# Optimization experiments

Measured on AMD Instinct MI355X. Metric: run time of the kernel, lower is better.

The kernel has to match this reference:

```python
import jax, jax.numpy as jnp
import numpy as np


def setup_inputs() -> dict:
    key = jax.random.key(0)
    kx, kc = jax.random.split(key)
    N, K, D = 32768, 4096, 512
    x = jax.random.normal(kx, (N, D), dtype=jnp.float32)
    # matches torch.rand(K, D) * 0.2 - 0.1
    codebook = jax.random.uniform(kc, (K, D), dtype=jnp.float32) * 0.2 - 0.1
    return {"x": x, "codebook": codebook}


def reference(x, codebook):
    x_sq = jnp.sum(x * x, axis=-1, keepdims=True)            # [N, 1]
    c_sq = jnp.sum(codebook * codebook, axis=-1)             # [K]
    dists = x_sq - 2.0 * jnp.einsum('nd,kd->nk', x, codebook) + c_sq[None, :]
    Z = jnp.argmin(dists, axis=-1)                           # [N] int
    q = codebook[Z]                                          # [N, D] gather
    q_with_st = x + jax.lax.stop_gradient(q - x)             # straight-through
    vq_loss = jnp.mean((jax.lax.stop_gradient(q) - x) ** 2)
    commitment_loss = jnp.mean((jax.lax.stop_gradient(x) - q) ** 2)
    return Z, q_with_st, vq_loss, commitment_loss
```

## Files before the change

kernel.cpp:

```cpp
#include <hip/hip_runtime.h>

static constexpr int N = 32768;
static constexpr int K = 4096;
static constexpr int D = 512;

typedef _Float16 f16x8 __attribute__((ext_vector_type(8)));
typedef float f32x4 __attribute__((ext_vector_type(4)));

#define GLD16(GP, LP)                                                   \
  __builtin_amdgcn_global_load_lds(                                     \
      (const __attribute__((address_space(1))) void*)(GP),              \
      (__attribute__((address_space(3))) void*)(LP), 16, 0, 0)

__global__ __launch_bounds__(256) void rowsq_convert_kernel(
    const float* __restrict__ in, float* __restrict__ sqout,
    _Float16* __restrict__ hi, float scale, int rows) {
  __shared__ float ls[8][512];
  int rb = blockIdx.x * 8;
  int tid = threadIdx.x;
#pragma unroll
  for (int g2 = 0; g2 < 2; ++g2) {
    int g = g2 * 256 + tid;
    int r = g >> 6;
    int c8 = (g & 63) * 8;
    const float4* p = (const float4*)(in + (size_t)(rb + r) * D + c8);
    float4 a = p[0], b = p[1];
    float s[8] = {a.x, a.y, a.z, a.w, b.x, b.y, b.z, b.w};
    union { _Float16 h[8]; f16x8 v; } H;
#pragma unroll
    for (int jj = 0; jj < 8; ++jj) {
      H.h[jj] = (_Float16)(s[jj] * scale);
      ls[r][c8 + jj] = s[jj];
    }
    *(f16x8*)(hi + (size_t)(rb + r) * D + c8) = H.v;
  }
  __syncthreads();
  int rr = tid >> 5;
  int l = tid & 31;
  const float* p = &ls[rr][(l >> 3) * 128 + (l & 7)];
  float r = 0.f;
#pragma unroll
  for (int i = 0; i < 16; ++i) {
    float v = p[i * 8];
    r = __fadd_rn(r, __fmul_rn(v, v));
  }
  r = __fadd_rn(r, __shfl_xor(r, 1));
  r = __fadd_rn(r, __shfl_xor(r, 2));
  r = __fadd_rn(r, __shfl_xor(r, 4));
  r = __fadd_rn(r, __shfl_xor(r, 8));
  r = __fadd_rn(r, __shfl_xor(r, 16));
  if (l == 0) sqout[rb + rr] = r;
}

__global__ __launch_bounds__(256) void transpose_kernel(
    const float* __restrict__ in, float* __restrict__ outT) {
  __shared__ float t[32][33];
  int bk = blockIdx.x;
  int bd = blockIdx.y;
  int tx = threadIdx.x, ty = threadIdx.y;
#pragma unroll
  for (int j = 0; j < 32; j += 8)
    t[ty + j][tx] = in[(size_t)(bk * 32 + ty + j) * D + bd * 32 + tx];
  __syncthreads();
#pragma unroll
  for (int j = 0; j < 32; j += 8)
    outT[(size_t)(bd * 32 + ty + j) * K + bk * 32 + tx] = t[tx][ty + j];
}

__global__ __launch_bounds__(256) void mfma_argmin_kernel(
    const _Float16* __restrict__ xh, const _Float16* __restrict__ ch,
    const float* __restrict__ xsq, const float* __restrict__ csq,
    float* __restrict__ pv1, int* __restrict__ pi1, float* __restrict__ pv2) {
  __shared__ __align__(16) _Float16 Bh[2][128 * 32];
  __shared__ float mbv1[128];
  __shared__ int mbi1[128];
  __shared__ float mbv2[128];

  int bid = blockIdx.x;
  int xcd = bid & 7, j = bid >> 3;
  int rowPanel = xcd * 32 + (j >> 5);
  int colPanel = j & 31;

  int tid = threadIdx.x;
  int w = tid >> 6, l = tid & 63;
  int wr = w >> 1, wc = w & 1;
  int wrow = wr * 64, wcol = wc * 64;
  int rA = l & 15, g = l >> 4;

  const size_t rowBase = (size_t)rowPanel * 128;
  const size_t colBase = (size_t)colPanel * 128;

  f32x4 acc[4][4];
#pragma unroll
  for (int mi = 0; mi < 4; ++mi)
#pragma unroll
    for (int ni = 0; ni < 4; ++ni) acc[mi][ni] = (f32x4)0.f;

  const int r0 = tid >> 2, s0 = tid & 3;
  const int cs = s0 ^ ((r0 >> 1) & 3);
  const int swz = (g ^ ((rA >> 1) & 3)) * 8;
  const _Float16* bSrc = ch + (colBase + r0) * D + cs * 8;

  auto stageB = [&](int buf, int kt) {
    const int dOff = kt * 32;
    GLD16(bSrc + dOff, &Bh[buf][(size_t)tid * 8]);
    GLD16(bSrc + dOff + (size_t)64 * D, &Bh[buf][(size_t)(tid + 256) * 8]);
  };

  const _Float16* aRow[4];
#pragma unroll
  for (int f = 0; f < 4; ++f)
    aRow[f] = xh + (rowBase + wrow + f * 16 + rA) * D + g * 8;

  f16x8 aCur[4], aNext[4];
  stageB(0, 0);
#pragma unroll
  for (int f = 0; f < 4; ++f) aCur[f] = *(const f16x8*)(aRow[f]);

  int cur = 0;
#pragma unroll
  for (int kt = 0; kt < 16; ++kt) {
    __syncthreads();
    if (kt < 15) {
      stageB(cur ^ 1, kt + 1);
#pragma unroll
      for (int f = 0; f < 4; ++f)
        aNext[f] = *(const f16x8*)(aRow[f] + (kt + 1) * 32);
    }
    f16x8 bh[4];
#pragma unroll
    for (int f = 0; f < 4; ++f)
      bh[f] = *(const f16x8*)&Bh[cur][(wcol + f * 16 + rA) * 32 + swz];
#pragma unroll
    for (int mi = 0; mi < 4; ++mi)
#pragma unroll
      for (int ni = 0; ni < 4; ++ni)
        acc[mi][ni] =
            __builtin_amdgcn_mfma_f32_16x16x32_f16(aCur[mi], bh[ni], acc[mi][ni], 0, 0, 0);
    if (kt < 15) {
#pragma unroll
      for (int f = 0; f < 4; ++f) aCur[f] = aNext[f];
    }
    cur ^= 1;
  }

  const float inv2048 = 1.0f / 2048.0f;
  float fv1[4][4], fv2[4][4];
  int fi1[4][4];
#pragma unroll
  for (int mi = 0; mi < 4; ++mi) {
#pragma unroll
    for (int r = 0; r < 4; ++r) {
      int row_l = wrow + mi * 16 + g * 4 + r;
      float xq = xsq[rowBase + row_l];
      float bv1 = 1e30f, bv2 = 1e30f;
      int bi1 = 0x7fffffff;
#pragma unroll
      for (int ni = 0; ni < 4; ++ni) {
        int col = (int)colBase + wcol + ni * 16 + rA;
        float S = acc[mi][ni][r];
        float dsc = (xq - S * inv2048) + csq[col];
        if (dsc < bv1 || (dsc == bv1 && col < bi1)) {
          bv2 = bv1; bv1 = dsc; bi1 = col;
        } else if (dsc < bv2) {
          bv2 = dsc;
        }
      }
#pragma unroll
      for (int m = 1; m < 16; m <<= 1) {
        float ov1 = __shfl_xor(bv1, m);
        int oi1 = __shfl_xor(bi1, m);
        float ov2 = __shfl_xor(bv2, m);
        if (ov1 < bv1 || (ov1 == bv1 && oi1 < bi1)) {
          bv2 = fminf(bv1, ov2); bv1 = ov1; bi1 = oi1;
        } else {
          bv2 = fminf(bv2, ov1);
        }
      }
      fv1[mi][r] = bv1; fv2[mi][r] = bv2; fi1[mi][r] = bi1;
      if (wc == 1 && rA == 0) {
        mbv1[row_l] = bv1; mbi1[row_l] = bi1; mbv2[row_l] = bv2;
      }
    }
  }
  __syncthreads();
  if (wc == 0 && rA == 0) {
#pragma unroll
    for (int mi = 0; mi < 4; ++mi) {
#pragma unroll
      for (int r = 0; r < 4; ++r) {
        int row_l = wrow + mi * 16 + g * 4 + r;
        float bv1 = fv1[mi][r], bv2 = fv2[mi][r];
        int bi1 = fi1[mi][r];
        float ov1 = mbv1[row_l];
        int oi1 = mbi1[row_l];
        float ov2 = mbv2[row_l];
        if (ov1 < bv1 || (ov1 == bv1 && oi1 < bi1)) {
          bv2 = fminf(bv1, ov2); bv1 = ov1; bi1 = oi1;
        } else {
          bv2 = fminf(bv2, ov1);
        }
        size_t o = (size_t)colPanel * N + (rowBase + row_l);
        pv1[o] = bv1; pi1[o] = bi1; pv2[o] = bv2;
      }
    }
  }
}

__global__ __launch_bounds__(256) void reduce_kernel(
    const float* __restrict__ pv1, const int* __restrict__ pi1,
    const float* __restrict__ pv2, float* __restrict__ zout,
    int* __restrict__ ctr, int* __restrict__ list, float eps) {
  int row = blockIdx.x * 256 + threadIdx.x;
  if (row >= N) return;
  float v1 = 1e30f, v2 = 1e30f;
  int i1 = 0x7fffffff;
  for (int jj = 0; jj < 32; ++jj) {
    float ov1 = pv1[(size_t)jj * N + row];
    float ov2 = pv2[(size_t)jj * N + row];
    int oi1 = pi1[(size_t)jj * N + row];
    if (ov1 < v1 || (ov1 == v1 && oi1 < i1)) {
      v2 = fminf(v1, ov2); v1 = ov1; i1 = oi1;
    } else {
      v2 = fminf(v2, ov1);
    }
  }
  zout[row] = (float)i1;
  if (v2 - v1 < eps) {
    int p = atomicAdd(ctr, 1);
    if (p < N) list[p] = row;
  }
}

static constexpr int RT_ROWS = 16;
static constexpr int RT_PANELS = 8;
static constexpr int CHUNK_D = 8;

__global__ __launch_bounds__(256) void rescore_tiled_kernel(
    const float* __restrict__ x, const float* __restrict__ cbT,
    const float* __restrict__ xsq, const float* __restrict__ csq,
    const int* __restrict__ ctr, const int* __restrict__ list,
    float* __restrict__ prv, int* __restrict__ pri) {
  __shared__ float xs[RT_ROWS][D + 4];
  __shared__ __align__(16) float cbs[2][CHUNK_D][512];
  int cnt = *ctr;
  if (cnt > N) cnt = N;
  int nTiles = (cnt + RT_ROWS - 1) / RT_ROWS;
  int nItems = nTiles * RT_PANELS;
  int tid = threadIdx.x;
  int ty = tid >> 4;
  int tx = tid & 15;

  for (int item = blockIdx.x; item < nItems; item += gridDim.x) {
    int tileIdx = item >> 3;
    int panel = item & 7;
    int base = tileIdx * RT_ROWS;
    int colPanel = panel * 512;
    __syncthreads();

    for (int i = tid; i < RT_ROWS * (D / 4); i += 256) {
      int r = i >> 7;
      int d4 = i & 127;
      int fi = base + r;
      int row = list[fi < cnt ? fi : 0];
      ((float4*)&xs[r][0])[d4] = ((const float4*)(x + (size_t)row * D))[d4];
    }

    auto stageCb = [&](int buf, int chk) {
      const float* src = cbT + (size_t)(chk * CHUNK_D) * K + colPanel;
#pragma unroll
      for (int it = 0; it < 4; ++it) {
        int f = it * 256 + tid;
        int dd = f >> 7, c4 = f & 127;
        GLD16(src + (size_t)dd * K + c4 * 4, &cbs[buf][0][0] + (size_t)f * 4);
      }
    };

    stageCb(0, 0);
    float acc[32];
#pragma unroll
    for (int c = 0; c < 32; ++c) acc[c] = 0.f;

    int cur = 0;
    for (int chk = 0; chk < D / CHUNK_D; ++chk) {
      __syncthreads();
      if (chk < D / CHUNK_D - 1) stageCb(cur ^ 1, chk + 1);
#pragma unroll
      for (int dd = 0; dd < CHUNK_D; ++dd) {
        float xa = xs[ty][chk * CHUNK_D + dd];
        const float4* cp = (const float4*)&cbs[cur][dd][0];
#pragma unroll
        for (int jj = 0; jj < 8; ++jj) {
          float4 v = cp[tx + jj * 16];
          acc[jj * 4 + 0] = fmaf(xa, v.x, acc[jj * 4 + 0]);
          acc[jj * 4 + 1] = fmaf(xa, v.y, acc[jj * 4 + 1]);
          acc[jj * 4 + 2] = fmaf(xa, v.z, acc[jj * 4 + 2]);
          acc[jj * 4 + 3] = fmaf(xa, v.w, acc[jj * 4 + 3]);
        }
      }
      cur ^= 1;
    }

    int fi = base + ty;
    int row = list[fi < cnt ? fi : 0];
    float xq = xsq[row];
    float bv = 1e30f;
    int bi = 0x7fffffff;
#pragma unroll
    for (int jj = 0; jj < 8; ++jj) {
#pragma unroll
      for (int q = 0; q < 4; ++q) {
        int col = colPanel + jj * 64 + tx * 4 + q;
        float a = acc[jj * 4 + q];
        float two = __fadd_rn(a, a);
        float t = __fsub_rn(xq, two);
        float dsc = __fadd_rn(t, csq[col]);
        if (dsc < bv || (dsc == bv && col < bi)) { bv = dsc; bi = col; }
      }
    }
#pragma unroll
    for (int m = 1; m < 16; m <<= 1) {
      float ov = __shfl_xor(bv, m);
      int oi = __shfl_xor(bi, m);
      if (ov < bv || (ov == bv && oi < bi)) { bv = ov; bi = oi; }
    }
    if (tx == 0 && fi < cnt) {
      prv[(size_t)fi * RT_PANELS + panel] = bv;
      pri[(size_t)fi * RT_PANELS + panel] = bi;
    }
  }
}

__global__ __launch_bounds__(256) void rescore_reduce_kernel(
    const float* __restrict__ prv, const int* __restrict__ pri,
    const int* __restrict__ ctr, const int* __restrict__ list,
    float* __restrict__ zout) {
  int cnt = *ctr;
  if (cnt > N) cnt = N;
  for (int fi = blockIdx.x * 256 + threadIdx.x; fi < cnt;
       fi += gridDim.x * 256) {
    float bv = 1e30f;
    int bi = 0x7fffffff;
#pragma unroll
    for (int p = 0; p < RT_PANELS; ++p) {
      float v = prv[(size_t)fi * RT_PANELS + p];
      int i = pri[(size_t)fi * RT_PANELS + p];
      if (v < bv || (v == bv && i < bi)) { bv = v; bi = i; }
    }
    zout[list[fi]] = (float)bi;
  }
}

static constexpr int BM = 64;
static constexpr int BKc = 128;
static constexpr int BD = 32;

__global__ __launch_bounds__(256) void argmin_fp32_kernel(
    const float* __restrict__ x, const float* __restrict__ cb,
    const float* __restrict__ xsq, const float* __restrict__ csq,
    float* __restrict__ zout) {
  __shared__ float xs[BD][BM];
  __shared__ float cs_[BD][BKc];
  __shared__ float mv[BM][16];
  __shared__ int mi[BM][16];

  int tid = threadIdx.x;
  int tx = tid & 15;
  int ty = tid >> 4;
  int row0 = blockIdx.x * BM;

  float bestv[4];
  int besti[4];
  float xsqr[4];
#pragma unroll
  for (int i = 0; i < 4; ++i) {
    bestv[i] = 3.4e38f;
    besti[i] = 0x7fffffff;
    xsqr[i] = xsq[row0 + ty * 4 + i];
  }

  for (int kt = 0; kt < K; kt += BKc) {
    float acc[4][8];
#pragma unroll
    for (int i = 0; i < 4; ++i)
#pragma unroll
      for (int jj = 0; jj < 8; ++jj) acc[i][jj] = 0.f;

    for (int dt = 0; dt < D; dt += BD) {
      __syncthreads();
      {
        int r = tid >> 2, d0 = (tid & 3) * 8;
        const float* src = x + (size_t)(row0 + r) * D + dt + d0;
        float4 v0 = *(const float4*)(src);
        float4 v1 = *(const float4*)(src + 4);
        xs[d0 + 0][r] = v0.x; xs[d0 + 1][r] = v0.y;
        xs[d0 + 2][r] = v0.z; xs[d0 + 3][r] = v0.w;
        xs[d0 + 4][r] = v1.x; xs[d0 + 5][r] = v1.y;
        xs[d0 + 6][r] = v1.z; xs[d0 + 7][r] = v1.w;
      }
      {
        int kk = tid >> 1, d0 = (tid & 1) * 16;
        const float* src = cb + (size_t)(kt + kk) * D + dt + d0;
        float4 v0 = *(const float4*)(src);
        float4 v1 = *(const float4*)(src + 4);
        float4 v2 = *(const float4*)(src + 8);
        float4 v3 = *(const float4*)(src + 12);
        cs_[d0 + 0][kk] = v0.x;  cs_[d0 + 1][kk] = v0.y;
        cs_[d0 + 2][kk] = v0.z;  cs_[d0 + 3][kk] = v0.w;
        cs_[d0 + 4][kk] = v1.x;  cs_[d0 + 5][kk] = v1.y;
        cs_[d0 + 6][kk] = v1.z;  cs_[d0 + 7][kk] = v1.w;
        cs_[d0 + 8][kk] = v2.x;  cs_[d0 + 9][kk] = v2.y;
        cs_[d0 + 10][kk] = v2.z; cs_[d0 + 11][kk] = v2.w;
        cs_[d0 + 12][kk] = v3.x; cs_[d0 + 13][kk] = v3.y;
        cs_[d0 + 14][kk] = v3.z; cs_[d0 + 15][kk] = v3.w;
      }
      __syncthreads();
#pragma unroll 4
      for (int d = 0; d < BD; ++d) {
        float xa[4], cv[8];
        *(float4*)&xa[0] = *(const float4*)&xs[d][ty * 4];
        *(float4*)&cv[0] = *(const float4*)&cs_[d][tx * 8];
        *(float4*)&cv[4] = *(const float4*)&cs_[d][tx * 8 + 4];
#pragma unroll
        for (int i = 0; i < 4; ++i)
#pragma unroll
          for (int jj = 0; jj < 8; ++jj)
            acc[i][jj] = fmaf(xa[i], cv[jj], acc[i][jj]);
      }
    }

#pragma unroll
    for (int jj = 0; jj < 8; ++jj) {
      int k = kt + tx * 8 + jj;
      float cq = csq[k];
#pragma unroll
      for (int i = 0; i < 4; ++i) {
        float two = __fadd_rn(acc[i][jj], acc[i][jj]);
        float t = __fsub_rn(xsqr[i], two);
        float dsc = __fadd_rn(t, cq);
        if (dsc < bestv[i]) { bestv[i] = dsc; besti[i] = k; }
      }
    }
  }

  __syncthreads();
#pragma unroll
  for (int i = 0; i < 4; ++i) {
    mv[ty * 4 + i][tx] = bestv[i];
    mi[ty * 4 + i][tx] = besti[i];
  }
  __syncthreads();
  if (tid < BM) {
    float bv = mv[tid][0];
    int bi = mi[tid][0];
#pragma unroll
    for (int t = 1; t < 16; ++t) {
      float v = mv[tid][t];
      int ii = mi[tid][t];
      if (v < bv || (v == bv && ii < bi)) { bv = v; bi = ii; }
    }
    zout[row0 + tid] = (float)bi;
  }
}

__global__ __launch_bounds__(256) void gather_kernel(
    const float* __restrict__ x, const float* __restrict__ cb,
    const float* __restrict__ zf, float* __restrict__ qout,
    float* __restrict__ partial) {
  __shared__ float red[256];
  const size_t TOT4 = (size_t)N * D / 4;
  size_t t0 = (size_t)blockIdx.x * 256 + threadIdx.x;
  float lsum = 0.f;
  for (size_t f = t0; f < TOT4; f += (size_t)2048 * 256) {
    int n = (int)(f >> 7);
    int d4 = (int)(f & 127);
    int z = (int)zf[n];
    float4 xv = ((const float4*)x)[f];
    float4 qv = *(const float4*)(cb + (size_t)z * D + d4 * 4);
    float dx0 = __fsub_rn(qv.x, xv.x);
    float dx1 = __fsub_rn(qv.y, xv.y);
    float dx2 = __fsub_rn(qv.z, xv.z);
    float dx3 = __fsub_rn(qv.w, xv.w);
    float4 o;
    o.x = __fadd_rn(xv.x, dx0);
    o.y = __fadd_rn(xv.y, dx1);
    o.z = __fadd_rn(xv.z, dx2);
    o.w = __fadd_rn(xv.w, dx3);
    ((float4*)qout)[f] = o;
    lsum += dx0 * dx0 + dx1 * dx1 + dx2 * dx2 + dx3 * dx3;
  }
  red[threadIdx.x] = lsum;
  __syncthreads();
  for (int s = 128; s > 0; s >>= 1) {
    if (threadIdx.x < s) red[threadIdx.x] += red[threadIdx.x + s];
    __syncthreads();
  }
  if (threadIdx.x == 0) partial[blockIdx.x] = red[0];
}

__global__ __launch_bounds__(256) void loss_kernel(const float* __restrict__ partial,
                                                   float* __restrict__ loss_out) {
  __shared__ float red[256];
  float s = 0.f;
  for (int i = threadIdx.x; i < 2048; i += 256) s += partial[i];
  red[threadIdx.x] = s;
  __syncthreads();
  for (int k = 128; k > 0; k >>= 1) {
    if (threadIdx.x < k) red[threadIdx.x] += red[threadIdx.x + k];
    __syncthreads();
  }
  if (threadIdx.x == 0) {
    float m = red[0] / (float)((size_t)N * D);
    loss_out[0] = m;
    loss_out[1] = m;
  }
}

static constexpr size_t OFF_XSQ = 0;
static constexpr size_t OFF_CSQ = 131072;
static constexpr size_t OFF_PART = 147456;
static constexpr size_t OFF_CTR = 155648;
static constexpr size_t OFF_LIST = 155904;
static constexpr size_t OFF_PV1 = 286976;
static constexpr size_t OFF_PI1 = OFF_PV1 + 4194304;
static constexpr size_t OFF_PV2 = OFF_PI1 + 4194304;
static constexpr size_t OFF_PRV = OFF_PV2 + 4194304;
static constexpr size_t OFF_PRI = OFF_PRV + 1048576;
static constexpr size_t WS_REQ = OFF_PRI + 1048576;

extern "C" void kernel_launch(void* const* d_in, const int* in_sizes, int n_in,
                              void* d_out, int out_size, void* d_ws, size_t ws_size,
                              hipStream_t stream) {
  const float* x = (const float*)d_in[0];
  const float* cb = (const float*)d_in[1];
  float* out = (float*)d_out;

  float* zout = out;
  float* qout = out + N;
  float* lout = out + N + (size_t)N * D;

  char* ws = (char*)d_ws;
  float* xsq = (float*)(ws + OFF_XSQ);
  float* csq = (float*)(ws + OFF_CSQ);
  float* partial = (float*)(ws + OFF_PART);

  _Float16* xhi = (_Float16*)qout;
  float* cbT = (float*)((char*)qout + (size_t)N * D * 2);
  _Float16* chi = (_Float16*)((char*)cbT + (size_t)D * K * 4);

  rowsq_convert_kernel<<<dim3(N / 8), dim3(256), 0, stream>>>(x, xsq, xhi,
                                                              16.0f, N);
  rowsq_convert_kernel<<<dim3(K / 8), dim3(256), 0, stream>>>(cb, csq, chi,
                                                              256.0f, K);

  if (ws_size >= WS_REQ) {
    int* ctr = (int*)(ws + OFF_CTR);
    int* list = (int*)(ws + OFF_LIST);
    float* pv1 = (float*)(ws + OFF_PV1);
    int* pi1 = (int*)(ws + OFF_PI1);
    float* pv2 = (float*)(ws + OFF_PV2);
    float* prv = (float*)(ws + OFF_PRV);
    int* pri = (int*)(ws + OFF_PRI);

    transpose_kernel<<<dim3(K / 32, D / 32), dim3(32, 8), 0, stream>>>(cb, cbT);
    hipMemsetAsync(ctr, 0, sizeof(int), stream);
    mfma_argmin_kernel<<<dim3((N / 128) * (K / 128)), dim3(256), 0, stream>>>(
        xhi, chi, xsq, csq, pv1, pi1, pv2);
    reduce_kernel<<<dim3(N / 256), dim3(256), 0, stream>>>(pv1, pi1, pv2, zout,
                                                           ctr, list, 0.02f);
    rescore_tiled_kernel<<<dim3(1024), dim3(256), 0, stream>>>(
        x, cbT, xsq, csq, ctr, list, prv, pri);
    rescore_reduce_kernel<<<dim3(128), dim3(256), 0, stream>>>(prv, pri, ctr,
                                                               list, zout);
  } else {
    argmin_fp32_kernel<<<dim3(N / BM), dim3(256), 0, stream>>>(x, cb, xsq, csq,
                                                               zout);
  }

  gather_kernel<<<dim3(2048), dim3(256), 0, stream>>>(x, cb, zout, qout, partial);
  loss_kernel<<<dim3(1), dim3(256), 0, stream>>>(partial, lout);
}
```

Before: 644.8 us.

## Stage A tiles through LDS with triple-buffered async prefetch pipeline

The A operand (x rows) is no longer loaded directly from global memory into registers. It is now staged through LDS with global_load_lds, like B. Both operands use a three-deep LDS ring with a prefetch distance of two, manual vmcnt waits and one barrier per k-step instead of a full __syncthreads. This is meant to hide global latency better and cut per-wave register pressure and redundant A loads, at the cost of tripling LDS use (which may lower occupancy) and relying on hand-tuned wait counts.

```diff
diff --git a/kernel.cpp b/kernel.cpp
--- a/kernel.cpp
+++ b/kernel.cpp
@@ -11,6 +11,8 @@
   __builtin_amdgcn_global_load_lds(                                     \
       (const __attribute__((address_space(1))) void*)(GP),              \
       (__attribute__((address_space(3))) void*)(LP), 16, 0, 0)
+
+#define SCHED_FENCE __builtin_amdgcn_sched_barrier(0)
 
 __global__ __launch_bounds__(256) void rowsq_convert_kernel(
     const float* __restrict__ in, float* __restrict__ sqout,
@@ -71,7 +73,8 @@
     const _Float16* __restrict__ xh, const _Float16* __restrict__ ch,
     const float* __restrict__ xsq, const float* __restrict__ csq,
     float* __restrict__ pv1, int* __restrict__ pi1, float* __restrict__ pv2) {
-  __shared__ __align__(16) _Float16 Bh[2][128 * 32];
+  __shared__ __align__(16) _Float16 Ah[3][128 * 32];
+  __shared__ __align__(16) _Float16 Bh[3][128 * 32];
   __shared__ float mbv1[128];
   __shared__ int mbi1[128];
   __shared__ float mbv2[128];
@@ -99,49 +102,49 @@
   const int r0 = tid >> 2, s0 = tid & 3;
   const int cs = s0 ^ ((r0 >> 1) & 3);
   const int swz = (g ^ ((rA >> 1) & 3)) * 8;
+
+  const _Float16* aSrc = xh + (rowBase + r0) * D + cs * 8;
   const _Float16* bSrc = ch + (colBase + r0) * D + cs * 8;
 
-  auto stageB = [&](int buf, int kt) {
+  auto stage = [&](int buf, int kt) {
     const int dOff = kt * 32;
+    GLD16(aSrc + dOff, &Ah[buf][(size_t)tid * 8]);
+    GLD16(aSrc + dOff + (size_t)64 * D, &Ah[buf][(size_t)(tid + 256) * 8]);
     GLD16(bSrc + dOff, &Bh[buf][(size_t)tid * 8]);
     GLD16(bSrc + dOff + (size_t)64 * D, &Bh[buf][(size_t)(tid + 256) * 8]);
   };
 
-  const _Float16* aRow[4];
-#pragma unroll
-  for (int f = 0; f < 4; ++f)
-    aRow[f] = xh + (rowBase + wrow + f * 16 + rA) * D + g * 8;
-
-  f16x8 aCur[4], aNext[4];
-  stageB(0, 0);
-#pragma unroll
-  for (int f = 0; f < 4; ++f) aCur[f] = *(const f16x8*)(aRow[f]);
-
-  int cur = 0;
+  stage(0, 0);
+  SCHED_FENCE;
+  stage(1, 1);
+  SCHED_FENCE;
+
 #pragma unroll
   for (int kt = 0; kt < 16; ++kt) {
-    __syncthreads();
-    if (kt < 15) {
-      stageB(cur ^ 1, kt + 1);
-#pragma unroll
-      for (int f = 0; f < 4; ++f)
-        aNext[f] = *(const f16x8*)(aRow[f] + (kt + 1) * 32);
-    }
-    f16x8 bh[4];
-#pragma unroll
-    for (int f = 0; f < 4; ++f)
+    if (kt == 15) {
+      asm volatile("s_waitcnt vmcnt(0)" ::: "memory");
+    } else {
+      asm volatile("s_waitcnt vmcnt(4)" ::: "memory");
+    }
+    SCHED_FENCE;
+    __builtin_amdgcn_s_barrier();
+    SCHED_FENCE;
+    const int cur = kt % 3;
+    if (kt < 14) stage((kt + 2) % 3, kt + 2);
+    SCHED_FENCE;
+
+    f16x8 ah[4], bh[4];
+#pragma unroll
+    for (int f = 0; f < 4; ++f) {
+      ah[f] = *(const f16x8*)&Ah[cur][(wrow + f * 16 + rA) * 32 + swz];
       bh[f] = *(const f16x8*)&Bh[cur][(wcol + f * 16 + rA) * 32 + swz];
+    }
 #pragma unroll
     for (int mi = 0; mi < 4; ++mi)
 #pragma unroll
       for (int ni = 0; ni < 4; ++ni)
         acc[mi][ni] =
-            __builtin_amdgcn_mfma_f32_16x16x32_f16(aCur[mi], bh[ni], acc[mi][ni], 0, 0, 0);
-    if (kt < 15) {
-#pragma unroll
-      for (int f = 0; f < 4; ++f) aCur[f] = aNext[f];
-    }
-    cur ^= 1;
+            __builtin_amdgcn_mfma_f32_16x16x32_f16(ah[mi], bh[ni], acc[mi][ni], 0, 0, 0);
   }
 
   const float inv2048 = 1.0f / 2048.0f;
```

Measured after the change: 618.0 us. 4.1% less time.
